# Kernel optimization log

Measured on AMD Instinct MI355X. Metric: run time of the kernel, lower is better.

## Reference

```python
import jax, jax.numpy as jnp
from jax import lax
import numpy as np

D_IN = 512    # inputdim
HID = 128     # hiddendim
D_INNER = 2 * HID   # 256
D_PROJ = 2 * D_INNER  # 512
N_STATE = 16
R_DT = 8      # ceil(128/16)
B, H, W = 8, 32, 32


def _layernorm(y, g, b):
    mu = y.mean(-1, keepdims=True)
    var = ((y - mu) ** 2).mean(-1, keepdims=True)
    return (y - mu) / jnp.sqrt(var + 1e-5) * g + b


def _ssm(x, xw, dtw, dtb, Al, Dv, g, be):
    # x: [B, D, L] -> y: [B, L, D]  (Mamba selective scan, delta_softplus=True)
    Bb, D, L = x.shape
    n = Al.shape[1]
    xd = jnp.einsum('bdl,kd->blk', x, xw)             # [B,L,R+2N]
    dts = xd[..., :R_DT]
    Bs = xd[..., R_DT:R_DT + n]                        # [B,L,N]
    Cs = xd[..., R_DT + n:]                            # [B,L,N]
    delta = jax.nn.softplus(jnp.einsum('blr,dr->bld', dts, dtw) + dtb)  # [B,L,D]
    A = -jnp.exp(Al)                                   # [D,N]
    xt = x.transpose(0, 2, 1)                          # [B,L,D]
    dA = jnp.exp(delta[..., None] * A)                 # [B,L,D,N]
    dBx = delta[..., None] * Bs[:, :, None, :] * xt[..., None]  # [B,L,D,N]

    def step(h, inp):
        da, dbx, c = inp
        h = h * da + dbx
        return h, jnp.einsum('bdn,bn->bd', h, c)

    h0 = jnp.zeros((Bb, D, n), x.dtype)
    _, ys = lax.scan(step, h0, (dA.transpose(1, 0, 2, 3),
                                dBx.transpose(1, 0, 2, 3),
                                Cs.transpose(1, 0, 2)))
    y = ys.transpose(1, 0, 2) + xt * Dv                # [B,L,D]
    return _layernorm(y, g, be)


def _up2(y, h, w):
    Bb, L, C = y.shape
    img = y.transpose(0, 2, 1).reshape(Bb, C, h, w)
    img = jnp.repeat(jnp.repeat(img, 2, axis=2), 2, axis=3)
    return img.reshape(Bb, C, 4 * L).transpose(0, 2, 1)


def _conv1x1(x, w, b):
    return jnp.einsum('bchw,oc->bohw', x, w) + b[None, :, None, None]


def _conv2s2(x, w, b):
    out = lax.conv_general_dilated(x, w, (2, 2), 'VALID',
                                   dimension_numbers=('NCHW', 'OIHW', 'NCHW'))
    return out + b[None, :, None, None]


def _forward(input_f, in_w, in_b, c1_w, c1_b, c2_w, c2_b, c3_w, c3_b, out_w, out_b,
             xw1, dtw1, dtb1, Al1, Dv1, g1, be1,
             xw2, dtw2, dtb2, Al2, Dv2, g2, be2,
             xw3, dtw3, dtb3, Al3, Dv3, g3, be3):
    xz = _conv1x1(input_f, in_w, in_b)
    x, z = jnp.split(xz, 2, axis=1)
    f1 = _conv1x1(x, c1_w, c1_b)                      # [B,256,H,W]
    f2 = _conv2s2(f1, c2_w, c2_b)                     # [B,256,H/2,W/2]
    f3 = _conv2s2(f2, c3_w, c3_b)                     # [B,256,H/4,W/4]

    Bb, C, h3, w3 = f3.shape
    fx3 = f3.reshape(Bb, C, h3 * w3)
    y3 = _ssm(fx3, xw3, dtw3, dtb3, Al3, Dv3, g3, be3) + \
         jnp.flip(_ssm(jnp.flip(fx3, -1), xw3, dtw3, dtb3, Al3, Dv3, g3, be3), 1)
    y2_ = _up2(y3, h3, w3)

    _, _, h2, w2 = f2.shape
    fx2 = f2.reshape(Bb, C, h2 * w2)
    y2 = _ssm(fx2, xw2, dtw2, dtb2, Al2, Dv2, g2, be2) + \
         jnp.flip(_ssm(jnp.flip(fx2, -1), xw2, dtw2, dtb2, Al2, Dv2, g2, be2), 1) + y2_
    y1_ = _up2(y2, h2, w2)

    _, _, h1, w1 = f1.shape
    fx1 = f1.reshape(Bb, C, h1 * w1)
    # NOTE: source uses fssm1 forward and fssm2 on the flipped sequence
    y1 = _ssm(fx1, xw1, dtw1, dtb1, Al1, Dv1, g1, be1) + \
         jnp.flip(_ssm(jnp.flip(fx1, -1), xw2, dtw2, dtb2, Al2, Dv2, g2, be2), 1) + y1_

    out1 = y1.transpose(0, 2, 1).reshape(Bb, C, h1, w1)
    out = out1 * jax.nn.silu(z)
    return _conv1x1(out, out_w, out_b)


def setup_inputs() -> dict:
    key = jax.random.key(0)
    ks = iter(jax.random.split(key, 64))
    def nrm(shape, s=0.05):
        return (jax.random.normal(next(ks), shape, dtype=jnp.float32) * s)
    inp = {
        'input_f': jax.random.normal(next(ks), (B, D_IN, H, W), dtype=jnp.float32),
        'in_w': nrm((D_PROJ, D_IN)), 'in_b': nrm((D_PROJ,)),
        'c1_w': nrm((D_INNER, D_INNER)), 'c1_b': nrm((D_INNER,)),
        'c2_w': nrm((D_INNER, D_INNER, 2, 2)), 'c2_b': nrm((D_INNER,)),
        'c3_w': nrm((D_INNER, D_INNER, 2, 2)), 'c3_b': nrm((D_INNER,)),
        'out_w': nrm((D_IN, D_INNER)), 'out_b': nrm((D_IN,)),
    }
    Al = jnp.log(jnp.tile(jnp.arange(1, N_STATE + 1, dtype=jnp.float32), (D_INNER, 1)))
    for i in (1, 2, 3):
        inp[f'xw{i}'] = nrm((R_DT + 2 * N_STATE, D_INNER))
        inp[f'dtw{i}'] = nrm((D_INNER, R_DT), s=R_DT ** -0.5)
        inp[f'dtb{i}'] = nrm((D_INNER,)) - 4.0   # inv-softplus of small dt
        inp[f'Al{i}'] = Al
        inp[f'Dv{i}'] = jnp.ones((D_INNER,), jnp.float32)
        inp[f'g{i}'] = jnp.ones((D_INNER,), jnp.float32)
        inp[f'be{i}'] = jnp.zeros((D_INNER,), jnp.float32)
    return inp


def reference(input_f, in_w, in_b, c1_w, c1_b, c2_w, c2_b, c3_w, c3_b, out_w, out_b,
              xw1, dtw1, dtb1, Al1, Dv1, g1, be1,
              xw2, dtw2, dtb2, Al2, Dv2, g2, be2,
              xw3, dtw3, dtb3, Al3, Dv3, g3, be3):
    return _forward(input_f, in_w, in_b, c1_w, c1_b, c2_w, c2_b, c3_w, c3_b, out_w, out_b,
                    xw1, dtw1, dtb1, Al1, Dv1, g1, be1,
                    xw2, dtw2, dtb2, Al2, Dv2, g2, be2,
                    xw3, dtw3, dtb3, Al3, Dv3, g3, be3)
```

## Files before the change

### kernel.cpp

```cpp
#include <hip/hip_runtime.h>
#include <cstddef>

#define DEV static __device__ __forceinline__

typedef __attribute__((ext_vector_type(8))) short short8;
typedef __attribute__((ext_vector_type(4))) float floatx4;

DEV float siluf(float v) { return v / (1.f + expf(-v)); }

DEV unsigned short f2bf(float f) {
  unsigned int u = __float_as_uint(f);
  u += 0x7fff + ((u >> 16) & 1);
  return (unsigned short)(u >> 16);
}
DEV float bf2f(unsigned short u) {
  return __uint_as_float(((unsigned int)u) << 16);
}
DEV float4 bf2f4(ushort4 v) {
  return make_float4(bf2f(v.x), bf2f(v.y), bf2f(v.z), bf2f(v.w));
}

template <int AMT>
DEV float ror_add(float v) {
  int s = __builtin_amdgcn_update_dpp(0, __float_as_int(v), 0x120 | AMT, 0xF, 0xF, false);
  return v + __int_as_float(s);
}

__global__ __launch_bounds__(256) void prep_k(
    const float* __restrict__ in_w, const float* __restrict__ c1_w,
    const float* __restrict__ c2_w, const float* __restrict__ c3_w,
    const float* __restrict__ out_w, const float* __restrict__ xw1,
    const float* __restrict__ xw2, const float* __restrict__ xw3,
    unsigned short* __restrict__ wsW,
    const float* __restrict__ input_f, unsigned short* __restrict__ inT)
{
  __shared__ float tile[32][33];
  int bid = blockIdx.x;
  int t = threadIdx.x;
  if (bid < 3960) {
    int gid = bid * 256 + t;
    float v;
    if      (gid < 262144)  v = in_w[gid];
    else if (gid < 327680)  v = c1_w[gid - 262144];
    else if (gid < 589824)  {
      int off = gid - 327680;
      int o = off >> 10, kk = off & 1023, ij = kk >> 8, c = kk & 255;
      v = c2_w[o * 1024 + c * 4 + ij];
    }
    else if (gid < 851968)  {
      int off = gid - 589824;
      int o = off >> 10, kk = off & 1023, ij = kk >> 8, c = kk & 255;
      v = c3_w[o * 1024 + c * 4 + ij];
    }
    else if (gid < 983040)  v = out_w[gid - 851968];
    else if (gid < 993280)  v = xw1[gid - 983040];
    else if (gid < 1003520) v = xw2[gid - 993280];
    else                    v = xw3[gid - 1003520];
    wsW[gid] = f2bf(v);
  } else {
    int idx = bid - 3960;
    int b = idx >> 9, blk = idx & 511;
    int pt = blk & 31, ct = blk >> 5;
    int p0 = pt * 32, c0 = ct * 32;
    int r = t >> 5, cc = t & 31;
#pragma unroll
    for (int i = 0; i < 4; i++) {
      int row = r + 8 * i;
      tile[row][cc] = input_f[((size_t)b * 512 + c0 + row) * 1024 + p0 + cc];
    }
    __syncthreads();
#pragma unroll
    for (int i = 0; i < 4; i++) {
      int row = r + 8 * i;
      inT[((size_t)b * 1024 + p0 + row) * 512 + c0 + cc] = f2bf(tile[cc][row]);
    }
  }
}

template <int EPI>
DEV void mgemm_body(const unsigned short* __restrict__ A, long long sA,
                    const unsigned short* __restrict__ B, long long sB,
                    const float* __restrict__ bias,
                    void* __restrict__ O1, void* __restrict__ O2,
                    int M, int N, int K, int Mt, int Nt, int bid)
{
  __shared__ __align__(16) unsigned short Ab[128 * 40];
  __shared__ __align__(16) unsigned short Bb[128 * 40];
  int tiles = Mt * Nt;
  int bb = bid / tiles;
  int rr = bid - bb * tiles;
  int m0 = (rr / Nt) * 128;
  int n0 = (rr % Nt) * 128;
  const unsigned short* Ap = A + (size_t)bb * sA;
  const unsigned short* Bp = B + (size_t)bb * sB;

  int t = threadIdx.x;
  int lane = t & 63;
  int wm = ((t >> 7) & 1) * 64;
  int wn = ((t >> 6) & 1) * 64;
  int l15 = lane & 15, quad = lane >> 4;

  int srow = t >> 1;
  int shalf = (t & 1) * 16;
  int arow = m0 + srow; if (arow > M - 1) arow = M - 1;
  int brow = n0 + srow; if (brow > N - 1) brow = N - 1;
  const unsigned short* ap = Ap + (size_t)arow * K + shalf;
  const unsigned short* bp = Bp + (size_t)brow * K + shalf;
  unsigned short* as = &Ab[srow * 40 + shalf];
  unsigned short* bs = &Bb[srow * 40 + shalf];

  floatx4 acc[4][4] = {};

  for (int k0 = 0; k0 < K; k0 += 32) {
    uint4 a0 = *(const uint4*)(ap + k0);
    uint4 a1 = *(const uint4*)(ap + k0 + 8);
    uint4 b0 = *(const uint4*)(bp + k0);
    uint4 b1 = *(const uint4*)(bp + k0 + 8);
    __syncthreads();
    *(uint4*)as = a0; *(uint4*)(as + 8) = a1;
    *(uint4*)bs = b0; *(uint4*)(bs + 8) = b1;
    __syncthreads();
    short8 af[4], bf[4];
#pragma unroll
    for (int i = 0; i < 4; i++)
      af[i] = *(const short8*)&Ab[(wm + i * 16 + l15) * 40 + quad * 8];
#pragma unroll
    for (int j = 0; j < 4; j++)
      bf[j] = *(const short8*)&Bb[(wn + j * 16 + l15) * 40 + quad * 8];
#pragma unroll
    for (int i = 0; i < 4; i++)
#pragma unroll
      for (int j = 0; j < 4; j++)
        acc[i][j] = __builtin_amdgcn_mfma_f32_16x16x32_bf16(af[i], bf[j],
                                                            acc[i][j], 0, 0, 0);
  }

  if (EPI == 1) {
    unsigned short* Yt = (unsigned short*)O1;
    unsigned short* Ys = (unsigned short*)O2;
    float bn[4]; int nn[4];
#pragma unroll
    for (int j = 0; j < 4; j++) { nn[j] = n0 + wn + j * 16 + l15; bn[j] = bias[nn[j]]; }
#pragma unroll
    for (int i = 0; i < 4; i++) {
      int pixb = m0 + wm + i * 16 + quad * 4;
#pragma unroll
      for (int j = 0; j < 4; j++) {
        int n = nn[j];
        if (n < 256) {
#pragma unroll
          for (int r = 0; r < 4; r++)
            Yt[((size_t)bb * 1024 + pixb + r) * 256 + n] = f2bf(acc[i][j][r] + bn[j]);
        } else {
#pragma unroll
          for (int r = 0; r < 4; r++)
            Ys[((size_t)bb * 1024 + pixb + r) * 256 + (n - 256)] =
                f2bf(siluf(acc[i][j][r] + bn[j]));
        }
      }
    }
  } else {
#pragma unroll
    for (int i = 0; i < 4; i++) {
      int m = m0 + wm + i * 16 + quad * 4;
#pragma unroll
      for (int j = 0; j < 4; j++) {
        int n = n0 + wn + j * 16 + l15;
        if (m < M && n < N) {
          float vr[4];
#pragma unroll
          for (int r = 0; r < 4; r++)
            vr[r] = acc[i][j][r] + (bias ? bias[m + r] : 0.f);
          if (EPI == 0) {
            float* Y0 = (float*)O1;
            float* yp = &Y0[((size_t)bb * M + m) * N + n];
#pragma unroll
            for (int r = 0; r < 4; r++) yp[(size_t)r * N] = vr[r];
          } else {
            unsigned short* Y0b = (unsigned short*)O1;
            unsigned short* Yt  = (unsigned short*)O2;
#pragma unroll
            for (int r = 0; r < 4; r++)
              Y0b[((size_t)bb * M + m + r) * N + n] = f2bf(vr[r]);
            ushort4 o;
            o.x = f2bf(vr[0]); o.y = f2bf(vr[1]); o.z = f2bf(vr[2]); o.w = f2bf(vr[3]);
            *(ushort4*)&Yt[((size_t)bb * N + n) * M + m] = o;
          }
        }
      }
    }
  }
}

template <int EPI>
__global__ __launch_bounds__(256) void mgemm_k(
    const unsigned short* __restrict__ A, long long sA,
    const unsigned short* __restrict__ B, long long sB,
    const float* __restrict__ bias, void* __restrict__ O1, void* __restrict__ O2,
    int M, int N, int K, int Mt, int Nt)
{
  mgemm_body<EPI>(A, sA, B, sB, bias, O1, O2, M, N, K, Mt, Nt, blockIdx.x);
}

__global__ __launch_bounds__(256) void fat1_k(
    const unsigned short* __restrict__ w_xw12, const unsigned short* __restrict__ f1t,
    float* __restrict__ xd12, unsigned short* __restrict__ ic2)
{
  int bid = blockIdx.x;
  if (bid < 64) {
    mgemm_body<0>(w_xw12, 0, f1t, 1024 * 256, nullptr, xd12, nullptr,
                  80, 1024, 256, 1, 8, bid);
  } else {
    int idx = (bid - 64) * 256 + threadIdx.x;
    int cs = idx & 31, ij = (idx >> 5) & 3, n = (idx >> 7) & 255, b = idx >> 15;
    int i = ij >> 1, j = ij & 1;
    int y = n >> 4, x = n & 15;
    int pix = (2 * y + i) * 32 + 2 * x + j;
    uint4 v = *(const uint4*)&f1t[((size_t)b * 1024 + pix) * 256 + cs * 8];
    *(uint4*)&ic2[((size_t)b * 256 + n) * 1024 + ij * 256 + cs * 8] = v;
  }
}

__global__ __launch_bounds__(256) void fat2_k(
    const unsigned short* __restrict__ w_xw2, const unsigned short* __restrict__ f2t,
    float* __restrict__ xd2, unsigned short* __restrict__ ic3)
{
  int bid = blockIdx.x;
  if (bid < 16) {
    mgemm_body<0>(w_xw2, 0, f2t, 256 * 256, nullptr, xd2, nullptr,
                  40, 256, 256, 1, 2, bid);
  } else {
    int idx = (bid - 16) * 256 + threadIdx.x;
    int cs = idx & 31, ij = (idx >> 5) & 3, n = (idx >> 7) & 63, b = idx >> 13;
    int i = ij >> 1, j = ij & 1;
    int y = n >> 3, x = n & 7;
    int pix = (2 * y + i) * 16 + 2 * x + j;
    uint4 v = *(const uint4*)&f2t[((size_t)b * 256 + pix) * 256 + cs * 8];
    *(uint4*)&ic3[((size_t)b * 64 + n) * 1024 + ij * 256 + cs * 8] = v;
  }
}

__global__ __launch_bounds__(256) void post_all_k(
    const float* __restrict__ xd12, const float* __restrict__ xd2,
    const float* __restrict__ xd3,
    const float* __restrict__ dtw1, const float* __restrict__ dtb1,
    const float* __restrict__ dtw2, const float* __restrict__ dtb2,
    const float* __restrict__ dtw3, const float* __restrict__ dtb3,
    float* __restrict__ d1f, float* __restrict__ bc1f,
    float* __restrict__ d1b, float* __restrict__ bc1b,
    float* __restrict__ d2g, float* __restrict__ bc2,
    float* __restrict__ d3g, float* __restrict__ bc3)
{
  int bid = blockIdx.x;
  const float* xd; int bstride, L; const float *dtw, *dtb; float *dg, *bg;
  int lt, b;
  if (bid < 512) {
    int r = bid; lt = r & 63; b = r >> 6;
    xd = xd12; bstride = 80 * 1024; L = 1024; dtw = dtw1; dtb = dtb1; dg = d1f; bg = bc1f;
  } else if (bid < 1024) {
    int r = bid - 512; lt = r & 63; b = r >> 6;
    xd = xd12 + 40 * 1024; bstride = 80 * 1024; L = 1024; dtw = dtw2; dtb = dtb2; dg = d1b; bg = bc1b;
  } else if (bid < 1152) {
    int r = bid - 1024; lt = r & 15; b = r >> 4;
    xd = xd2; bstride = 40 * 256; L = 256; dtw = dtw2; dtb = dtb2; dg = d2g; bg = bc2;
  } else {
    int r = bid - 1152; lt = r & 3; b = r >> 2;
    xd = xd3; bstride = 40 * 64; L = 64; dtw = dtw3; dtb = dtb3; dg = d3g; bg = bc3;
  }
  int l0 = lt * 16;
  __shared__ float dl[8][16];
  int t = threadIdx.x;
  const float* xb = xd + (size_t)b * bstride + l0;
  if (t < 128) {
    int r = t >> 4, l = t & 15;
    dl[r][l] = xb[(size_t)r * L + l];
  } else {
    int tt = t - 128;
    int c = tt >> 2, seg = tt & 3;
    float4 v = *(const float4*)&xb[(size_t)(8 + c) * L + seg * 4];
    *(float4*)&bg[((size_t)b * 32 + c) * L + l0 + seg * 4] = v;
  }
  __syncthreads();
  int d = t;
  float dtwv[8];
#pragma unroll
  for (int r = 0; r < 8; r++) dtwv[r] = dtw[d * 8 + r];
  float dtbv = dtb[d];
  float spv[16];
#pragma unroll
  for (int l = 0; l < 16; l++) {
    float s = dtbv;
#pragma unroll
    for (int r = 0; r < 8; r++) s += dl[r][l] * dtwv[r];
    spv[l] = fmaxf(s, 0.f) + log1pf(expf(-fabsf(s)));
  }
  float* dout = dg + ((size_t)b * 256 + d) * L + l0;
#pragma unroll
  for (int i = 0; i < 4; i++)
    *(float4*)&dout[4 * i] = make_float4(spv[4 * i], spv[4 * i + 1],
                                         spv[4 * i + 2], spv[4 * i + 3]);
}

#define SCAN_STEPA(DVV, DXV, BVV) {                \
    float e_ = __expf((DVV) * A);                  \
    h = h * e_ + (BVV) * (DXV);                    \
    P *= e_; }

__global__ __launch_bounds__(256) void scanA_k(
    const unsigned short* __restrict__ f1b, const unsigned short* __restrict__ f2b,
    const float* __restrict__ d1f, const float* __restrict__ bc1f,
    const float* __restrict__ d1b, const float* __restrict__ bc1b,
    const float* __restrict__ d2,  const float* __restrict__ bc2,
    const float* __restrict__ Al1, const float* __restrict__ Al2,
    float* __restrict__ cP, float* __restrict__ cQ)
{
  __shared__ __align__(16) float lds[48][68];
  int bid = blockIdx.x;
  int sid, tseg, L; const unsigned short* xin; const float *dlp, *bcp, *Alp;
  if (bid < 4096) {
    sid = bid >> 4; tseg = bid & 15; L = 1024; xin = f1b;
    if (((sid >> 4) & 1) == 0) { dlp = d1f; bcp = bc1f; Alp = Al1; }
    else                       { dlp = d1b; bcp = bc1b; Alp = Al2; }
  } else {
    int idx = bid - 4096; sid = idx >> 2; tseg = idx & 3; L = 256;
    xin = f2b; dlp = d2; bcp = bc2; Alp = Al2;
  }
  int b = sid >> 5, dir = (sid >> 4) & 1, g = sid & 15;
  int t = threadIdx.x, n = t & 15, dloc = t >> 4, d = g * 16 + dloc;
  int mbase = dir ? (L - 64 * (tseg + 1)) : 64 * tseg;

  int r0 = t >> 4, cs = t & 15;
  {
    const float* p0 = dlp + ((size_t)b * 256 + g * 16 + r0) * L + mbase;
    const unsigned short* p1 = xin + ((size_t)b * 256 + g * 16 + r0) * L + mbase;
    const float* p2 = bcp + ((size_t)b * 32 + r0) * L + mbase;
    float4 v0 = *(const float4*)(p0 + cs * 4);
    float4 xf = bf2f4(*(const ushort4*)(p1 + cs * 4));
    float4 v2 = *(const float4*)(p2 + cs * 4);
    float4 dx = make_float4(v0.x * xf.x, v0.y * xf.y, v0.z * xf.z, v0.w * xf.w);
    *(float4*)&lds[r0][cs * 4]      = v0;
    *(float4*)&lds[16 + r0][cs * 4] = dx;
    *(float4*)&lds[32 + r0][cs * 4] = v2;
  }
  __syncthreads();

  float A = -expf(Alp[d * 16 + n]);
  float h = 0.f, P = 1.f;
  if (dir == 0) {
#pragma unroll
    for (int g4 = 0; g4 < 16; g4++) {
      int cb = 4 * g4;
      float4 dv4 = *(const float4*)&lds[dloc][cb];
      float4 dx4 = *(const float4*)&lds[16 + dloc][cb];
      float4 bv4 = *(const float4*)&lds[32 + n][cb];
      SCAN_STEPA(dv4.x, dx4.x, bv4.x);
      SCAN_STEPA(dv4.y, dx4.y, bv4.y);
      SCAN_STEPA(dv4.z, dx4.z, bv4.z);
      SCAN_STEPA(dv4.w, dx4.w, bv4.w);
    }
  } else {
#pragma unroll
    for (int g4 = 0; g4 < 16; g4++) {
      int cb = 60 - 4 * g4;
      float4 dv4 = *(const float4*)&lds[dloc][cb];
      float4 dx4 = *(const float4*)&lds[16 + dloc][cb];
      float4 bv4 = *(const float4*)&lds[32 + n][cb];
      SCAN_STEPA(dv4.w, dx4.w, bv4.w);
      SCAN_STEPA(dv4.z, dx4.z, bv4.z);
      SCAN_STEPA(dv4.y, dx4.y, bv4.y);
      SCAN_STEPA(dv4.x, dx4.x, bv4.x);
    }
  }
  cP[(size_t)bid * 256 + t] = P;
  cQ[(size_t)bid * 256 + t] = h;
}

#define SCAN_STEPY(DVV, DXV, BVV, CVV, COL) {      \
    float e_ = __expf((DVV) * A);                  \
    h = h * e_ + (BVV) * (DXV);                    \
    float pp_ = h * (CVV);                         \
    pp_ = ror_add<1>(pp_);                         \
    pp_ = ror_add<2>(pp_);                         \
    pp_ = ror_add<4>(pp_);                         \
    pp_ = ror_add<8>(pp_);                         \
    ysel = (((COL) & 15) == n) ? pp_ : ysel; }

__global__ __launch_bounds__(256) void scanC_k(
    const unsigned short* __restrict__ f1b, const unsigned short* __restrict__ f2b,
    const unsigned short* __restrict__ f3b,
    const float* __restrict__ d1f, const float* __restrict__ bc1f,
    const float* __restrict__ d1b, const float* __restrict__ bc1b,
    const float* __restrict__ d2,  const float* __restrict__ bc2,
    const float* __restrict__ d3,  const float* __restrict__ bc3,
    float* __restrict__ y1f, float* __restrict__ y1b,
    float* __restrict__ y2f, float* __restrict__ y2b,
    float* __restrict__ y3f, float* __restrict__ y3b,
    const float* __restrict__ Al1, const float* __restrict__ Dv1,
    const float* __restrict__ Al2, const float* __restrict__ Dv2,
    const float* __restrict__ Al3, const float* __restrict__ Dv3,
    const float* __restrict__ cP, const float* __restrict__ cQ)
{
  __shared__ __align__(16) float lds[64][68];
  int bid = blockIdx.x;
  int sid, tseg, L, sbase; const unsigned short* xin;
  const float *dlp, *bcp, *Alp, *Dvp; float* yo;
  if (bid < 4096) {
    sid = bid >> 4; tseg = bid & 15; sbase = sid * 16; L = 1024; xin = f1b;
    if (((sid >> 4) & 1) == 0) { dlp = d1f; bcp = bc1f; Alp = Al1; Dvp = Dv1; yo = y1f; }
    else                       { dlp = d1b; bcp = bc1b; Alp = Al2; Dvp = Dv2; yo = y1b; }
  } else if (bid < 5120) {
    int idx = bid - 4096; sid = idx >> 2; tseg = idx & 3; sbase = 4096 + sid * 4;
    L = 256; xin = f2b; dlp = d2; bcp = bc2; Alp = Al2; Dvp = Dv2;
    yo = ((sid >> 4) & 1) ? y2b : y2f;
  } else {
    sid = bid - 5120; tseg = 0; sbase = -1; L = 64;
    xin = f3b; dlp = d3; bcp = bc3; Alp = Al3; Dvp = Dv3;
    yo = ((sid >> 4) & 1) ? y3b : y3f;
  }
  int b = sid >> 5, dir = (sid >> 4) & 1, g = sid & 15;
  int t = threadIdx.x, n = t & 15, dloc = t >> 4, d = g * 16 + dloc;
  int mbase = dir ? (L - 64 * (tseg + 1)) : 64 * tseg;

  int r0 = t >> 4, cs = t & 15;
  {
    const float* p0 = dlp + ((size_t)b * 256 + g * 16 + r0) * L + mbase;
    const unsigned short* p1 = xin + ((size_t)b * 256 + g * 16 + r0) * L + mbase;
    const float* p2 = bcp + ((size_t)b * 32 + r0) * L + mbase;
    const float* p3 = bcp + ((size_t)b * 32 + 16 + r0) * L + mbase;
    float4 v0 = *(const float4*)(p0 + cs * 4);
    float4 xf = bf2f4(*(const ushort4*)(p1 + cs * 4));
    float4 v2 = *(const float4*)(p2 + cs * 4);
    float4 v3 = *(const float4*)(p3 + cs * 4);
    float4 dx = make_float4(v0.x * xf.x, v0.y * xf.y, v0.z * xf.z, v0.w * xf.w);
    *(float4*)&lds[r0][cs * 4]      = v0;
    *(float4*)&lds[16 + r0][cs * 4] = dx;
    *(float4*)&lds[32 + r0][cs * 4] = v2;
    *(float4*)&lds[48 + r0][cs * 4] = v3;
  }
  float A   = -expf(Alp[d * 16 + n]);
  float Dvv = Dvp[d];
  float h = 0.f;
  if (sbase >= 0) {
    for (int s = 0; s < tseg; ++s) {
      size_t off = (size_t)(sbase + s) * 256 + t;
      h = cP[off] * h + cQ[off];
    }
  }
  __syncthreads();

  float* ybase = yo + ((size_t)b * L + mbase) * 256 + d;
#pragma unroll
  for (int jj0 = 0; jj0 < 64; jj0 += 16) {
    float ysel = 0.f;
    if (dir == 0) {
#pragma unroll
      for (int g4 = 0; g4 < 4; g4++) {
        int cb = jj0 + 4 * g4;
        float4 dv4 = *(const float4*)&lds[dloc][cb];
        float4 dx4 = *(const float4*)&lds[16 + dloc][cb];
        float4 bv4 = *(const float4*)&lds[32 + n][cb];
        float4 cv4 = *(const float4*)&lds[48 + n][cb];
        SCAN_STEPY(dv4.x, dx4.x, bv4.x, cv4.x, cb + 0);
        SCAN_STEPY(dv4.y, dx4.y, bv4.y, cv4.y, cb + 1);
        SCAN_STEPY(dv4.z, dx4.z, bv4.z, cv4.z, cb + 2);
        SCAN_STEPY(dv4.w, dx4.w, bv4.w, cv4.w, cb + 3);
      }
    } else {
#pragma unroll
      for (int g4 = 0; g4 < 4; g4++) {
        int cb = 60 - jj0 - 4 * g4;
        float4 dv4 = *(const float4*)&lds[dloc][cb];
        float4 dx4 = *(const float4*)&lds[16 + dloc][cb];
        float4 bv4 = *(const float4*)&lds[32 + n][cb];
        float4 cv4 = *(const float4*)&lds[48 + n][cb];
        SCAN_STEPY(dv4.w, dx4.w, bv4.w, cv4.w, cb + 3);
        SCAN_STEPY(dv4.z, dx4.z, bv4.z, cv4.z, cb + 2);
        SCAN_STEPY(dv4.y, dx4.y, bv4.y, cv4.y, cb + 1);
        SCAN_STEPY(dv4.x, dx4.x, bv4.x, cv4.x, cb + 0);
      }
    }
    int colbase = dir ? 48 - jj0 : jj0;
    float dsel  = lds[dloc][colbase + n];
    float dxsel = lds[16 + dloc][colbase + n];
    float xsel  = dxsel / fmaxf(dsel, 1e-30f);
    ybase[(size_t)(colbase + n) * 256] = ysel + xsel * Dvv;
  }
}

template <int OUTBF>
__global__ __launch_bounds__(256) void ln_combine(
    const float* __restrict__ yf, const float* __restrict__ yb,
    const float* __restrict__ gf, const float* __restrict__ bef,
    const float* __restrict__ gb, const float* __restrict__ beb,
    const float* __restrict__ up, int Wc,
    const unsigned short* __restrict__ szb, void* __restrict__ outv,
    int L, int Wf)
{
  int bid = blockIdx.x;
  int b = bid / L;
  int l = bid - b * L;
  int d = threadIdx.x;
  size_t base = ((size_t)b * L + l) * 256 + d;
  float vf = yf[base], vb = yb[base];
  float4 s = make_float4(vf, vf * vf, vb, vb * vb);
#pragma unroll
  for (int m = 1; m < 64; m <<= 1) {
    s.x += __shfl_xor(s.x, m);
    s.y += __shfl_xor(s.y, m);
    s.z += __shfl_xor(s.z, m);
    s.w += __shfl_xor(s.w, m);
  }
  __shared__ float red[4][4];
  int w = threadIdx.x >> 6;
  if ((threadIdx.x & 63) == 0) {
    red[w][0] = s.x; red[w][1] = s.y; red[w][2] = s.z; red[w][3] = s.w;
  }
  __syncthreads();
  float s0 = red[0][0] + red[1][0] + red[2][0] + red[3][0];
  float s1 = red[0][1] + red[1][1] + red[2][1] + red[3][1];
  float s2 = red[0][2] + red[1][2] + red[2][2] + red[3][2];
  float s3 = red[0][3] + red[1][3] + red[2][3] + red[3][3];
  const float inv = 1.f / 256.f;
  float muf = s0 * inv, varf = s1 * inv - muf * muf;
  float mub = s2 * inv, varb = s3 * inv - mub * mub;
  float rf = rsqrtf(varf + 1e-5f);
  float rb = rsqrtf(varb + 1e-5f);
  float v = (vf - muf) * rf * gf[d] + bef[d] + (vb - mub) * rb * gb[d] + beb[d];
  if (up) {
    int y = l / Wf, x = l - y * Wf;
    int lc = (y >> 1) * Wc + (x >> 1);
    v += up[((size_t)b * (L >> 2) + lc) * 256 + d];
  }
  if (szb) v *= bf2f(szb[base]);
  if (OUTBF) ((unsigned short*)outv)[base] = f2bf(v);
  else       ((float*)outv)[base] = v;
}

extern "C" void kernel_launch(void* const* d_in, const int* in_sizes, int n_in,
                              void* d_out, int out_size, void* d_ws, size_t ws_size,
                              hipStream_t stream) {
  (void)in_sizes; (void)n_in; (void)out_size; (void)ws_size;
  const float* input_f = (const float*)d_in[0];
  const float* in_w  = (const float*)d_in[1];
  const float* in_b  = (const float*)d_in[2];
  const float* c1_w  = (const float*)d_in[3];
  const float* c1_b  = (const float*)d_in[4];
  const float* c2_w  = (const float*)d_in[5];
  const float* c2_b  = (const float*)d_in[6];
  const float* c3_w  = (const float*)d_in[7];
  const float* c3_b  = (const float*)d_in[8];
  const float* out_w = (const float*)d_in[9];
  const float* out_b = (const float*)d_in[10];
  const float* xw1  = (const float*)d_in[11];
  const float* dtw1 = (const float*)d_in[12];
  const float* dtb1 = (const float*)d_in[13];
  const float* Al1  = (const float*)d_in[14];
  const float* Dv1  = (const float*)d_in[15];
  const float* g1   = (const float*)d_in[16];
  const float* be1  = (const float*)d_in[17];
  const float* xw2  = (const float*)d_in[18];
  const float* dtw2 = (const float*)d_in[19];
  const float* dtb2 = (const float*)d_in[20];
  const float* Al2  = (const float*)d_in[21];
  const float* Dv2  = (const float*)d_in[22];
  const float* g2   = (const float*)d_in[23];
  const float* be2  = (const float*)d_in[24];
  const float* xw3  = (const float*)d_in[25];
  const float* dtw3 = (const float*)d_in[26];
  const float* dtb3 = (const float*)d_in[27];
  const float* Al3  = (const float*)d_in[28];
  const float* Dv3  = (const float*)d_in[29];
  const float* g3   = (const float*)d_in[30];
  const float* be3  = (const float*)d_in[31];

  float* ws = (float*)d_ws;
  constexpr size_t M1 = 2097152;
  float* d1f = ws;
  unsigned short* xt = (unsigned short*)(ws + M1);
  float* y1f = ws + M1;
  unsigned short* szb = (unsigned short*)(ws + 2 * M1);
  unsigned short* f1b = (unsigned short*)(ws + 3 * M1);
  unsigned short* G = (unsigned short*)(ws + 3 * M1) + 2097152;
  float* d1b = ws + 4 * M1;
  unsigned short* inT = (unsigned short*)(ws + 5 * M1);
  unsigned short* ic2 = inT;
  unsigned short* f1t = inT + 2097152;
  unsigned short* ic3 = f1t;
  float* y1b = ws + 5 * M1;
  size_t o = 6 * M1;
  unsigned short* f2b = (unsigned short*)(ws + o); o += 524288;
  unsigned short* f3b = (unsigned short*)(ws + o); o += 131072;
  float* bc1f = ws + o; o += 262144;
  float* bc1b = ws + o; o += 262144;
  float* d2   = ws + o; o += 524288;
  float* bc2  = ws + o; o += 65536;
  float* d3   = ws + o; o += 131072;
  float* bc3  = ws + o; o += 16384;
  float* y2f  = ws + o; o += 524288;
  float* y2b  = ws + o; o += 524288;
  float* y3f  = ws + o; o += 131072;
  float* y3b  = ws + o; o += 131072;
  float* y3c  = ws + o; o += 131072;
  float* y2c  = ws + o; o += 524288;
  float* cP   = ws + o; o += 1310720;
  float* cQ   = ws + o; o += 1310720;
  unsigned short* wsW = (unsigned short*)(ws + o); o += 506880;
  float* xd12 = cP;
  float* xd2  = cP + 655360;
  float* xd3  = cP + 737280;
  unsigned short* f2t = (unsigned short*)cQ;
  unsigned short* f3t = (unsigned short*)(cQ + 262144);
  unsigned short* w_in   = wsW;
  unsigned short* w_c1   = wsW + 262144;
  unsigned short* w_c2   = wsW + 327680;
  unsigned short* w_c3   = wsW + 589824;
  unsigned short* w_out  = wsW + 851968;
  unsigned short* w_xw12 = wsW + 983040;
  unsigned short* w_xw2  = wsW + 993280;
  unsigned short* w_xw3  = wsW + 1003520;

  dim3 blk(256);

  prep_k<<<dim3(8056), blk, 0, stream>>>(in_w, c1_w, c2_w, c3_w, out_w,
                                         xw1, xw2, xw3, wsW, input_f, inT);
  mgemm_k<1><<<dim3(256), blk, 0, stream>>>(inT, 1024 * 512, w_in, 0, in_b,
                                            xt, szb, 1024, 512, 512, 8, 4);
  mgemm_k<3><<<dim3(128), blk, 0, stream>>>(w_c1, 0, xt, 1024 * 256, c1_b,
                                            f1b, f1t, 256, 1024, 256, 2, 8);
  fat1_k<<<dim3(1088), blk, 0, stream>>>(w_xw12, f1t, xd12, ic2);
  mgemm_k<3><<<dim3(32), blk, 0, stream>>>(w_c2, 0, ic2, 256 * 1024, c2_b,
                                           f2b, f2t, 256, 256, 1024, 2, 2);
  fat2_k<<<dim3(272), blk, 0, stream>>>(w_xw2, f2t, xd2, ic3);
  mgemm_k<3><<<dim3(16), blk, 0, stream>>>(w_c3, 0, ic3, 64 * 1024, c3_b,
                                           f3b, f3t, 256, 64, 1024, 2, 1);
  mgemm_k<0><<<dim3(8), blk, 0, stream>>>(w_xw3, 0, f3t, 64 * 256, nullptr,
                                          xd3, nullptr, 40, 64, 256, 1, 1);
  post_all_k<<<dim3(1184), blk, 0, stream>>>(xd12, xd2, xd3,
                                             dtw1, dtb1, dtw2, dtb2, dtw3, dtb3,
                                             d1f, bc1f, d1b, bc1b, d2, bc2, d3, bc3);
  scanA_k<<<dim3(5120), blk, 0, stream>>>(f1b, f2b, d1f, bc1f, d1b, bc1b,
                                          d2, bc2, Al1, Al2, cP, cQ);
  scanC_k<<<dim3(5376), blk, 0, stream>>>(f1b, f2b, f3b,
                                          d1f, bc1f, d1b, bc1b, d2, bc2, d3, bc3,
                                          y1f, y1b, y2f, y2b, y3f, y3b,
                                          Al1, Dv1, Al2, Dv2, Al3, Dv3, cP, cQ);
  ln_combine<0><<<dim3(512), blk, 0, stream>>>(y3f, y3b, g3, be3, g3, be3,
                                               nullptr, 0, nullptr, y3c, 64, 8);
  ln_combine<0><<<dim3(2048), blk, 0, stream>>>(y2f, y2b, g2, be2, g2, be2,
                                                y3c, 8, nullptr, y2c, 256, 16);
  ln_combine<1><<<dim3(8192), blk, 0, stream>>>(y1f, y1b, g1, be1, g2, be2,
                                                y2c, 16, szb, G, 1024, 32);
  mgemm_k<0><<<dim3(256), blk, 0, stream>>>(w_out, 0, G, 1024 * 256, out_b,
                                            (float*)d_out, nullptr,
                                            512, 1024, 256, 4, 8);
}
```

Baseline: 375.8 us.

## Restructure scanC so each thread owns four states of one channel

```diff
diff --git a/kernel.cpp b/kernel.cpp
--- a/kernel.cpp
+++ b/kernel.cpp
@@ -20,9 +20,10 @@
   return make_float4(bf2f(v.x), bf2f(v.y), bf2f(v.z), bf2f(v.w));
 }
 
-template <int AMT>
-DEV float ror_add(float v) {
-  int s = __builtin_amdgcn_update_dpp(0, __float_as_int(v), 0x120 | AMT, 0xF, 0xF, false);
+template <int CTRL>
+DEV float qadd(float v) {
+  int s = __builtin_amdgcn_update_dpp(__float_as_int(v), __float_as_int(v),
+                                      CTRL, 0xF, 0xF, false);
   return v + __int_as_float(s);
 }
 
@@ -375,15 +376,28 @@
   cQ[(size_t)bid * 256 + t] = h;
 }
 
-#define SCAN_STEPY(DVV, DXV, BVV, CVV, COL) {      \
-    float e_ = __expf((DVV) * A);                  \
-    h = h * e_ + (BVV) * (DXV);                    \
-    float pp_ = h * (CVV);                         \
-    pp_ = ror_add<1>(pp_);                         \
-    pp_ = ror_add<2>(pp_);                         \
-    pp_ = ror_add<4>(pp_);                         \
-    pp_ = ror_add<8>(pp_);                         \
-    ysel = (((COL) & 15) == n) ? pp_ : ysel; }
+#define QSTEP(DS, XU, CI, II) {                                         \
+    float4 bv = *(const float4*)&ld_b[CI][n0];                          \
+    float4 cv = *(const float4*)&ld_c[CI][n0];                          \
+    float xs_ = bf2f(XU) * (DS);                                        \
+    float4 e_;                                                          \
+    e_.x = __builtin_amdgcn_exp2f((DS) * A4.x);                         \
+    e_.y = __builtin_amdgcn_exp2f((DS) * A4.y);                         \
+    e_.z = __builtin_amdgcn_exp2f((DS) * A4.z);                         \
+    e_.w = __builtin_amdgcn_exp2f((DS) * A4.w);                         \
+    h4.x = h4.x * e_.x + bv.x * xs_;                                    \
+    h4.y = h4.y * e_.y + bv.y * xs_;                                    \
+    h4.z = h4.z * e_.z + bv.z * xs_;                                    \
+    h4.w = h4.w * e_.w + bv.w * xs_;                                    \
+    float pp_ = h4.x * cv.x + h4.y * cv.y + h4.z * cv.z + h4.w * cv.w;  \
+    pp_ = qadd<0xB1>(pp_);                                              \
+    pp_ = qadd<0x4E>(pp_);                                              \
+    ysel = (nq == (II)) ? pp_ : ysel; }
+
+DEV float4 pcomb(float4 P, float4 h, float4 Q) {
+  return make_float4(P.x * h.x + Q.x, P.y * h.y + Q.y,
+                     P.z * h.z + Q.z, P.w * h.w + Q.w);
+}
 
 __global__ __launch_bounds__(256) void scanC_k(
     const unsigned short* __restrict__ f1b, const unsigned short* __restrict__ f2b,
@@ -400,90 +414,137 @@
     const float* __restrict__ Al3, const float* __restrict__ Dv3,
     const float* __restrict__ cP, const float* __restrict__ cQ)
 {
-  __shared__ __align__(16) float lds[64][68];
+  __shared__ __align__(16) float ld_d[64][68];
+  __shared__ __align__(16) unsigned short ld_xs[64][72];
+  __shared__ __align__(16) float ld_b[64][20];
+  __shared__ __align__(16) float ld_c[64][20];
+
   int bid = blockIdx.x;
-  int sid, tseg, L, sbase; const unsigned short* xin;
-  const float *dlp, *bcp, *Alp, *Dvp; float* yo;
-  if (bid < 4096) {
-    sid = bid >> 4; tseg = bid & 15; sbase = sid * 16; L = 1024; xin = f1b;
-    if (((sid >> 4) & 1) == 0) { dlp = d1f; bcp = bc1f; Alp = Al1; Dvp = Dv1; yo = y1f; }
-    else                       { dlp = d1b; bcp = bc1b; Alp = Al2; Dvp = Dv2; yo = y1b; }
-  } else if (bid < 5120) {
-    int idx = bid - 4096; sid = idx >> 2; tseg = idx & 3; sbase = 4096 + sid * 4;
-    L = 256; xin = f2b; dlp = d2; bcp = bc2; Alp = Al2; Dvp = Dv2;
-    yo = ((sid >> 4) & 1) ? y2b : y2f;
-  } else {
-    sid = bid - 5120; tseg = 0; sbase = -1; L = 64;
-    xin = f3b; dlp = d3; bcp = bc3; Alp = Al3; Dvp = Dv3;
-    yo = ((sid >> 4) & 1) ? y3b : y3f;
-  }
-  int b = sid >> 5, dir = (sid >> 4) & 1, g = sid & 15;
-  int t = threadIdx.x, n = t & 15, dloc = t >> 4, d = g * 16 + dloc;
+  int b, dir, g4, tseg, L, lvl;
+  const unsigned short* xin; const float *dlp, *bcp, *Alp, *Dvp; float* yo;
+  if (bid < 1024) {
+    b = bid >> 7; dir = (bid >> 6) & 1; g4 = (bid >> 4) & 3; tseg = bid & 15;
+    L = 1024; xin = f1b; lvl = 1;
+    if (dir == 0) { dlp = d1f; bcp = bc1f; Alp = Al1; Dvp = Dv1; yo = y1f; }
+    else          { dlp = d1b; bcp = bc1b; Alp = Al2; Dvp = Dv2; yo = y1b; }
+  } else if (bid < 1280) {
+    int idx = bid - 1024;
+    b = idx >> 5; dir = (idx >> 4) & 1; g4 = (idx >> 2) & 3; tseg = idx & 3;
+    L = 256; xin = f2b; lvl = 2;
+    dlp = d2; bcp = bc2; Alp = Al2; Dvp = Dv2; yo = dir ? y2b : y2f;
+  } else {
+    int idx = bid - 1280;
+    b = idx >> 3; dir = (idx >> 2) & 1; g4 = idx & 3; tseg = 0;
+    L = 64; xin = f3b; lvl = 3;
+    dlp = d3; bcp = bc3; Alp = Al3; Dvp = Dv3; yo = dir ? y3b : y3f;
+  }
   int mbase = dir ? (L - 64 * (tseg + 1)) : 64 * tseg;
-
-  int r0 = t >> 4, cs = t & 15;
+  int t = threadIdx.x;
+  int dl = t >> 2, nq = t & 3, n0 = nq * 4;
+  int d = g4 * 64 + dl;
+
   {
-    const float* p0 = dlp + ((size_t)b * 256 + g * 16 + r0) * L + mbase;
-    const unsigned short* p1 = xin + ((size_t)b * 256 + g * 16 + r0) * L + mbase;
-    const float* p2 = bcp + ((size_t)b * 32 + r0) * L + mbase;
-    const float* p3 = bcp + ((size_t)b * 32 + 16 + r0) * L + mbase;
-    float4 v0 = *(const float4*)(p0 + cs * 4);
-    float4 xf = bf2f4(*(const ushort4*)(p1 + cs * 4));
-    float4 v2 = *(const float4*)(p2 + cs * 4);
-    float4 v3 = *(const float4*)(p3 + cs * 4);
-    float4 dx = make_float4(v0.x * xf.x, v0.y * xf.y, v0.z * xf.z, v0.w * xf.w);
-    *(float4*)&lds[r0][cs * 4]      = v0;
-    *(float4*)&lds[16 + r0][cs * 4] = dx;
-    *(float4*)&lds[32 + r0][cs * 4] = v2;
-    *(float4*)&lds[48 + r0][cs * 4] = v3;
-  }
-  float A   = -expf(Alp[d * 16 + n]);
+    int rr = t >> 2, q = t & 3;
+    const float* dr = dlp + ((size_t)b * 256 + g4 * 64 + rr) * L + mbase;
+    const unsigned short* xr = xin + ((size_t)b * 256 + g4 * 64 + rr) * L + mbase;
+#pragma unroll
+    for (int j = 0; j < 4; ++j) {
+      int c = q * 4 + 16 * j;
+      float4 dv = *(const float4*)(dr + c);
+      ushort4 xu = *(const ushort4*)(xr + c);
+      *(float4*)&ld_d[rr][c] = dv;
+      *(ushort4*)&ld_xs[rr][c] = xu;
+    }
+    int nn = t >> 4, c4 = t & 15;
+    const float* br = bcp + ((size_t)b * 32 + nn) * L + mbase + c4 * 4;
+    const float* cr = br + (size_t)16 * L;
+    float4 bv = *(const float4*)br;
+    float4 cv = *(const float4*)cr;
+    ld_b[c4 * 4 + 0][nn] = bv.x; ld_b[c4 * 4 + 1][nn] = bv.y;
+    ld_b[c4 * 4 + 2][nn] = bv.z; ld_b[c4 * 4 + 3][nn] = bv.w;
+    ld_c[c4 * 4 + 0][nn] = cv.x; ld_c[c4 * 4 + 1][nn] = cv.y;
+    ld_c[c4 * 4 + 2][nn] = cv.z; ld_c[c4 * 4 + 3][nn] = cv.w;
+  }
+
+  float4 A4;
+  A4.x = -expf(Alp[d * 16 + n0 + 0]) * 1.442695040888963f;
+  A4.y = -expf(Alp[d * 16 + n0 + 1]) * 1.442695040888963f;
+  A4.z = -expf(Alp[d * 16 + n0 + 2]) * 1.442695040888963f;
+  A4.w = -expf(Alp[d * 16 + n0 + 3]) * 1.442695040888963f;
   float Dvv = Dvp[d];
-  float h = 0.f;
-  if (sbase >= 0) {
-    for (int s = 0; s < tseg; ++s) {
-      size_t off = (size_t)(sbase + s) * 256 + t;
-      h = cP[off] * h + cQ[off];
+
+  float4 h4 = make_float4(0.f, 0.f, 0.f, 0.f);
+  if (tseg > 0) {
+    int gold = g4 * 4 + (dl >> 4);
+    int soff = (lvl == 1) ? (b * 32 + dir * 16 + gold) * 16
+                          : 4096 + (b * 32 + dir * 16 + gold) * 4;
+    size_t cbase = (size_t)soff * 256 + (size_t)((dl & 15) * 16 + n0);
+    int s = 0;
+    for (; s + 4 <= tseg; s += 4) {
+      const float* p = &cP[cbase + (size_t)s * 256];
+      const float* q = &cQ[cbase + (size_t)s * 256];
+      float4 P0 = *(const float4*)(p);       float4 Q0 = *(const float4*)(q);
+      float4 P1 = *(const float4*)(p + 256); float4 Q1 = *(const float4*)(q + 256);
+      float4 P2 = *(const float4*)(p + 512); float4 Q2 = *(const float4*)(q + 512);
+      float4 P3 = *(const float4*)(p + 768); float4 Q3 = *(const float4*)(q + 768);
+      h4 = pcomb(P0, h4, Q0); h4 = pcomb(P1, h4, Q1);
+      h4 = pcomb(P2, h4, Q2); h4 = pcomb(P3, h4, Q3);
+    }
+    for (; s < tseg; ++s) {
+      float4 P = *(const float4*)&cP[cbase + (size_t)s * 256];
+      float4 Q = *(const float4*)&cQ[cbase + (size_t)s * 256];
+      h4 = pcomb(P, h4, Q);
     }
   }
   __syncthreads();
 
   float* ybase = yo + ((size_t)b * L + mbase) * 256 + d;
-#pragma unroll
-  for (int jj0 = 0; jj0 < 64; jj0 += 16) {
-    float ysel = 0.f;
-    if (dir == 0) {
-#pragma unroll
-      for (int g4 = 0; g4 < 4; g4++) {
-        int cb = jj0 + 4 * g4;
-        float4 dv4 = *(const float4*)&lds[dloc][cb];
-        float4 dx4 = *(const float4*)&lds[16 + dloc][cb];
-        float4 bv4 = *(const float4*)&lds[32 + n][cb];
-        float4 cv4 = *(const float4*)&lds[48 + n][cb];
-        SCAN_STEPY(dv4.x, dx4.x, bv4.x, cv4.x, cb + 0);
-        SCAN_STEPY(dv4.y, dx4.y, bv4.y, cv4.y, cb + 1);
-        SCAN_STEPY(dv4.z, dx4.z, bv4.z, cv4.z, cb + 2);
-        SCAN_STEPY(dv4.w, dx4.w, bv4.w, cv4.w, cb + 3);
+  if (dir == 0) {
+#pragma unroll
+    for (int p = 0; p < 4; ++p) {
+      float yk[4];
+#pragma unroll
+      for (int j = 0; j < 4; ++j) {
+        int cb = 16 * p + 4 * j;
+        float4 dv4 = *(const float4*)&ld_d[dl][cb];
+        ushort4 xu4 = *(const ushort4*)&ld_xs[dl][cb];
+        float ysel = 0.f;
+        QSTEP(dv4.x, xu4.x, cb + 0, 0);
+        QSTEP(dv4.y, xu4.y, cb + 1, 1);
+        QSTEP(dv4.z, xu4.z, cb + 2, 2);
+        QSTEP(dv4.w, xu4.w, cb + 3, 3);
+        yk[j] = ysel;
       }
-    } else {
-#pragma unroll
-      for (int g4 = 0; g4 < 4; g4++) {
-        int cb = 60 - jj0 - 4 * g4;
-        float4 dv4 = *(const float4*)&lds[dloc][cb];
-        float4 dx4 = *(const float4*)&lds[16 + dloc][cb];
-        float4 bv4 = *(const float4*)&lds[32 + n][cb];
-        float4 cv4 = *(const float4*)&lds[48 + n][cb];
-        SCAN_STEPY(dv4.w, dx4.w, bv4.w, cv4.w, cb + 3);
-        SCAN_STEPY(dv4.z, dx4.z, bv4.z, cv4.z, cb + 2);
-        SCAN_STEPY(dv4.y, dx4.y, bv4.y, cv4.y, cb + 1);
-        SCAN_STEPY(dv4.x, dx4.x, bv4.x, cv4.x, cb + 0);
+#pragma unroll
+      for (int j = 0; j < 4; ++j) {
+        int cst = 16 * p + 4 * j + nq;
+        float xv = bf2f(ld_xs[dl][cst]);
+        ybase[(size_t)cst * 256] = yk[j] + xv * Dvv;
       }
     }
-    int colbase = dir ? 48 - jj0 : jj0;
-    float dsel  = lds[dloc][colbase + n];
-    float dxsel = lds[16 + dloc][colbase + n];
-    float xsel  = dxsel / fmaxf(dsel, 1e-30f);
-    ybase[(size_t)(colbase + n) * 256] = ysel + xsel * Dvv;
+  } else {
+#pragma unroll
+    for (int p = 0; p < 4; ++p) {
+      float yk[4];
+#pragma unroll
+      for (int j = 0; j < 4; ++j) {
+        int cb = 60 - 16 * p - 4 * j;
+        float4 dv4 = *(const float4*)&ld_d[dl][cb];
+        ushort4 xu4 = *(const ushort4*)&ld_xs[dl][cb];
+        float ysel = 0.f;
+        QSTEP(dv4.w, xu4.w, cb + 3, 0);
+        QSTEP(dv4.z, xu4.z, cb + 2, 1);
+        QSTEP(dv4.y, xu4.y, cb + 1, 2);
+        QSTEP(dv4.x, xu4.x, cb + 0, 3);
+        yk[j] = ysel;
+      }
+#pragma unroll
+      for (int j = 0; j < 4; ++j) {
+        int cst = 60 - 16 * p - 4 * j + (3 - nq);
+        float xv = bf2f(ld_xs[dl][cst]);
+        ybase[(size_t)cst * 256] = yk[j] + xv * Dvv;
+      }
+    }
   }
 }
 
@@ -640,7 +701,7 @@
                                              d1f, bc1f, d1b, bc1b, d2, bc2, d3, bc3);
   scanA_k<<<dim3(5120), blk, 0, stream>>>(f1b, f2b, d1f, bc1f, d1b, bc1b,
                                           d2, bc2, Al1, Al2, cP, cQ);
-  scanC_k<<<dim3(5376), blk, 0, stream>>>(f1b, f2b, f3b,
+  scanC_k<<<dim3(1344), blk, 0, stream>>>(f1b, f2b, f3b,
                                           d1f, bc1f, d1b, bc1b, d2, bc2, d3, bc3,
                                           y1f, y1b, y2f, y2b, y3f, y3b,
                                           Al1, Dv1, Al2, Dv2, Al3, Dv3, cP, cQ);
```

Measured after the change: 368.1 us. 1.02x faster.
